# Performance work log

Hardware: AMD Instinct MI355X
Metric: run time of the kernel (lower is better)

The kernel has to match this reference:

```python
import jax, jax.numpy as jnp
import numpy as np


def _cheby_stack(xt, degree):
    # Note: this layer uses T1 = 2*tanh(x) (non-standard), recurrence T_n = 2*xt*T_{n-1} - T_{n-2}
    Ts = [jnp.ones_like(xt)]
    if degree > 0:
        Ts.append(2.0 * xt)
    for n in range(2, degree + 1):
        Ts.append(2.0 * xt * Ts[-1] - Ts[-2])
    return jnp.stack(Ts, axis=2)  # (b, p, n)


def _kan_layer(x, W, tW):
    deg = tW.shape[-1] - 1
    cheby = _cheby_stack(jnp.tanh(x), deg)  # (b, p, n)
    # Fused form of einsum('bpn,qpn->bqp') then einsum('bqp,qp->bq');
    # XLA contracts (tW*W) first, avoiding the huge (b,q,p) intermediate.
    return jnp.einsum('bpn,qpn,qp->bq', cheby, tW, W)


def _cheby_gelu(x, degree=5):
    # Here T1 = tanh(x) (standard), then GeLU(exact) of stacked basis, summed.
    xt = jnp.tanh(x)
    Ts = [jnp.ones_like(xt), xt]
    for n in range(2, degree + 1):
        Ts.append(2.0 * xt * Ts[-1] - Ts[-2])
    st = jnp.stack(Ts, axis=-1)
    return jax.nn.gelu(st, approximate=False).sum(axis=-1)


def setup_inputs() -> dict:
    key = jax.random.key(0)
    ks = jax.random.split(key, 12)
    batch, in_dim, mid, out_dim, deg = 131072, 8, 128, 1, 8
    nfeat = 32
    d = {}
    d['x'] = jax.random.normal(ks[0], (batch, in_dim), jnp.float32)
    d['B'] = jax.random.normal(ks[1], (in_dim, nfeat), jnp.float32)  # scale=1.0
    dims = [(mid, 2 * nfeat), (mid, mid), (mid, mid), (mid, mid), (out_dim, mid)]
    for i, (q, p) in enumerate(dims):
        std_W = np.sqrt(5.0 / (p + q)).astype(np.float32)
        std_tW = np.float32(1.0 / (deg + 1))
        d[f'W{i}'] = std_W * jax.random.normal(ks[2 + 2 * i], (q, p), jnp.float32)
        d[f'tW{i}'] = 0.1 + std_tW * jax.random.normal(ks[3 + 2 * i], (q, p, deg + 1), jnp.float32)
    return d


def reference(x, B, W0, tW0, W1, tW1, W2, tW2, W3, tW3, W4, tW4):
    # FourierFeatures
    proj = (2.0 * jnp.pi) * (x @ B)
    h = jnp.concatenate([jnp.sin(proj), jnp.cos(proj)], axis=-1)  # (b, 64)
    # KAN layers; dropout_prob=0.0 (eval) -> identity. Middle layers get residual
    h = _kan_layer(h, W0, tW0)
    h = _kan_layer(h, W1, tW1) + h
    h = _kan_layer(h, W2, tW2) + h
    h = _kan_layer(h, W3, tW3) + h
    h = _kan_layer(h, W4, tW4)  # (b, 1)
    return _cheby_gelu(h, degree=5)
```

## Files before the change

### kernel.cpp

```cpp
#include <hip/hip_runtime.h>

#define TPB 256

typedef _Float16 f16x8 __attribute__((ext_vector_type(8)));
typedef __fp16 h16x2 __attribute__((ext_vector_type(2)));
typedef float f32x4 __attribute__((ext_vector_type(4)));

static constexpr int WT_L0 = 0;
static constexpr int WT_L1 = 65536;
static constexpr int WT_L2 = 196608;
static constexpr int WT_L3 = 327680;
static constexpr int WT_END = 458752;
static constexpr int F32_BASE = WT_END;
static constexpr int MST = 132;

__device__ __forceinline__ float fast_tanh2(float x) {
  float e = __expf(2.0f * x);
  return fmaf(-4.0f, __builtin_amdgcn_rcpf(e + 1.0f), 2.0f);
}
__device__ __forceinline__ float gelu_exact(float v) {
  return 0.5f * v * (1.0f + erff(v * 0.70710678f));
}

__global__ void fuse_w_f16(const float* __restrict__ W, const float* __restrict__ tW,
                           _Float16* __restrict__ out_hi, _Float16* __restrict__ out_lo,
                           int P, int total, int sbits) {
  int i = blockIdx.x * 256 + threadIdx.x;
  if (i >= total) return;
  int j = i & 7, q = (i >> 3) & 15, g = (i >> 7) & 3, t = (i >> 9) & 7;
  int s = (i >> 12) & ((1 << sbits) - 1);
  int n1 = i >> (12 + sbits);
  int p = s * 32 + g * 8 + j;
  int qg = t * 16 + q;
  float v = tW[(qg * P + p) * 9 + (n1 + 1)] * W[qg * P + p];
  _Float16 hi = (_Float16)v;
  out_hi[i] = hi;
  out_lo[i] = (_Float16)(v - (float)hi);
}
__global__ void fuse_bias(const float* __restrict__ W, const float* __restrict__ tW,
                          float* __restrict__ bias, int P, int Q) {
  int q = blockIdx.x * 64 + threadIdx.x;
  if (q >= Q) return;
  float s = 0.0f;
  for (int p = 0; p < P; ++p) s += tW[(q * P + p) * 9] * W[q * P + p];
  bias[q] = s;
}
__global__ void fuse_w4(const float* __restrict__ W, const float* __restrict__ tW,
                        float* __restrict__ out) {
  int i = blockIdx.x * 128 + threadIdx.x;
  if (i >= 1152) return;
  out[i] = tW[i] * W[i / 9];
}

template <int S, bool RES>
__device__ __forceinline__ void layer_mfma(const float* __restrict__ mT,
                                           const _Float16* __restrict__ wt_hi,
                                           const _Float16* __restrict__ wt_lo,
                                           const float* __restrict__ biasL,
                                           f32x4 (&acc)[4][2], int l, int wq) {
  const int c15 = l & 15, g = l >> 4;
#pragma unroll
  for (int qt = 0; qt < 2; ++qt) {
    float bv = biasL[wq * 32 + qt * 16 + c15];
#pragma unroll
    for (int rt = 0; rt < 4; ++rt)
#pragma unroll
      for (int j = 0; j < 4; ++j) {
        if (RES) acc[rt][qt][j] += bv; else acc[rt][qt][j] = bv;
      }
  }
  const _Float16* slot_hi = wt_hi + wq * 1024 + l * 8;
  const _Float16* slot_lo = wt_lo + wq * 1024 + l * 8;
  float mv[4][8], up[4][8], uc[4][8];
  f16x8 bh0[2], bl0[2], bh1[2], bl1[2];

#define LB(dh, dl, ks)                                                        \
  {                                                                           \
    int s_ = (ks) >> 3, n_ = (ks) & 7;                                        \
    size_t off_ = (size_t)(n_ * S + s_) * 4096;                               \
    _Pragma("unroll") for (int qt = 0; qt < 2; ++qt) {                        \
      dh[qt] = *(const f16x8*)(slot_hi + off_ + qt * 512);                    \
      dl[qt] = *(const f16x8*)(slot_lo + off_ + qt * 512);                    \
    }                                                                         \
  }

#define AREAD(s_)                                                             \
  {                                                                           \
    _Pragma("unroll") for (int rt = 0; rt < 4; ++rt) {                        \
      const f32x4* mp_ =                                                      \
          (const f32x4*)(mT + (rt * 16 + c15) * MST + (s_) * 32 + g * 8);     \
      f32x4 a_ = mp_[0], b_ = mp_[1];                                         \
      _Pragma("unroll") for (int ii = 0; ii < 4; ++ii) {                      \
        mv[rt][ii] = a_[ii]; mv[rt][4 + ii] = b_[ii];                         \
      }                                                                       \
      _Pragma("unroll") for (int ii = 0; ii < 8; ++ii) {                      \
        up[rt][ii] = 1.0f; uc[rt][ii] = mv[rt][ii];                           \
      }                                                                       \
    }                                                                         \
  }

#define STEP(bh, bl)                                                          \
  {                                                                           \
    f16x8 afh[4], afl[4];                                                     \
    _Pragma("unroll") for (int rt = 0; rt < 4; ++rt) {                        \
      union U8 { h16x2 h2[4]; f16x8 v; } uh_, ul_;                            \
      _Pragma("unroll") for (int ii = 0; ii < 4; ++ii) {                      \
        float v0 = uc[rt][2 * ii], v1 = uc[rt][2 * ii + 1];                   \
        h16x2 h_ = __builtin_amdgcn_cvt_pkrtz(v0, v1);                        \
        uh_.h2[ii] = h_;                                                      \
        ul_.h2[ii] = __builtin_amdgcn_cvt_pkrtz(v0 - (float)h_[0],            \
                                                v1 - (float)h_[1]);           \
      }                                                                       \
      afh[rt] = uh_.v; afl[rt] = ul_.v;                                       \
    }                                                                         \
    _Pragma("unroll") for (int rt = 0; rt < 4; ++rt)                          \
      _Pragma("unroll") for (int ii = 0; ii < 8; ++ii) {                      \
        float u_ = fmaf(mv[rt][ii], uc[rt][ii], -up[rt][ii]);                 \
        up[rt][ii] = uc[rt][ii]; uc[rt][ii] = u_;                             \
      }                                                                       \
    _Pragma("unroll") for (int qt = 0; qt < 2; ++qt)                          \
      _Pragma("unroll") for (int rt = 0; rt < 4; ++rt)                        \
        acc[rt][qt] = __builtin_amdgcn_mfma_f32_16x16x32_f16(                 \
            afh[rt], bh[qt], acc[rt][qt], 0, 0, 0);                           \
    _Pragma("unroll") for (int qt = 0; qt < 2; ++qt)                          \
      _Pragma("unroll") for (int rt = 0; rt < 4; ++rt)                        \
        acc[rt][qt] = __builtin_amdgcn_mfma_f32_16x16x32_f16(                 \
            afl[rt], bh[qt], acc[rt][qt], 0, 0, 0);                           \
    _Pragma("unroll") for (int qt = 0; qt < 2; ++qt)                          \
      _Pragma("unroll") for (int rt = 0; rt < 4; ++rt)                        \
        acc[rt][qt] = __builtin_amdgcn_mfma_f32_16x16x32_f16(                 \
            afh[rt], bl[qt], acc[rt][qt], 0, 0, 0);                           \
  }

  LB(bh0, bl0, 0);
#pragma unroll 1
  for (int i = 0; i < 4 * S; ++i) {
    int ks = 2 * i;
    if ((ks & 7) == 0) AREAD(ks >> 3);
    LB(bh1, bl1, ks + 1);
    STEP(bh0, bl0);
    if (ks + 2 < 8 * S) LB(bh0, bl0, ks + 2);
    STEP(bh1, bl1);
  }
#undef LB
#undef AREAD
#undef STEP
}

__device__ __forceinline__ void write_m(float* __restrict__ mT,
                                        const f32x4 (&acc)[4][2], int l, int wq) {
  const int c15 = l & 15, g = l >> 4;
#pragma unroll
  for (int rt = 0; rt < 4; ++rt)
#pragma unroll
    for (int qt = 0; qt < 2; ++qt)
#pragma unroll
      for (int j = 0; j < 4; ++j) {
        int row = rt * 16 + g * 4 + j;
        int col = wq * 32 + qt * 16 + c15;
        mT[row * MST + col] = fast_tanh2(acc[rt][qt][j]);
      }
}

__global__ void __launch_bounds__(TPB, 2)
kan_mfma(const float* __restrict__ x, const float* __restrict__ Bm,
         const _Float16* __restrict__ wt_hi, const _Float16* __restrict__ wt_lo,
         const float* __restrict__ bias, const float* __restrict__ w4,
         float* __restrict__ out) {
  __shared__ float mT[64 * MST];
  int tid = threadIdx.x;
  int l = tid & 63;
  int wq = tid >> 6;
  int row0 = blockIdx.x * 64;

  {
    const float4* xp = (const float4*)(x + (size_t)(row0 + l) * 8);
    float4 a = xp[0], c4 = xp[1];
    float xv[8] = {a.x, a.y, a.z, a.w, c4.x, c4.y, c4.z, c4.w};
#pragma unroll
    for (int jj = 0; jj < 8; ++jj) {
      int j = wq * 8 + jj;
      float pr = 0.0f;
#pragma unroll
      for (int k = 0; k < 8; ++k) pr = fmaf(xv[k], Bm[k * 32 + j], pr);
      float ang = 6.2831853071795864f * pr;
      float sv, cv;
      sincosf(ang, &sv, &cv);
      mT[l * MST + j] = fast_tanh2(sv);
      mT[l * MST + 32 + j] = fast_tanh2(cv);
    }
  }
  __syncthreads();

  f32x4 acc[4][2];
  layer_mfma<2, false>(mT, wt_hi + WT_L0, wt_lo + WT_L0, bias + 0, acc, l, wq);
  __syncthreads();
  write_m(mT, acc, l, wq);
  __syncthreads();
  layer_mfma<4, true>(mT, wt_hi + WT_L1, wt_lo + WT_L1, bias + 128, acc, l, wq);
  __syncthreads();
  write_m(mT, acc, l, wq);
  __syncthreads();
  layer_mfma<4, true>(mT, wt_hi + WT_L2, wt_lo + WT_L2, bias + 256, acc, l, wq);
  __syncthreads();
  write_m(mT, acc, l, wq);
  __syncthreads();
  layer_mfma<4, true>(mT, wt_hi + WT_L3, wt_lo + WT_L3, bias + 384, acc, l, wq);
  __syncthreads();
  write_m(mT, acc, l, wq);
  __syncthreads();

  {
    int r16 = l & 15, pq = l >> 4;
    int r = wq * 16 + r16;
    const float* w4h = w4 + pq * 32 * 9;
    float part = 0.0f;
#pragma unroll 4
    for (int pp = 0; pp < 32; ++pp) {
      float mm = mT[r * MST + pq * 32 + pp];
      const float* wp = w4h + pp * 9;
      part += wp[0];
      part = fmaf(mm, wp[1], part);
      float u2 = 1.0f, u1 = mm;
#pragma unroll
      for (int n = 2; n < 9; ++n) {
        float u = fmaf(mm, u1, -u2);
        u2 = u1;
        u1 = u;
        part = fmaf(u, wp[n], part);
      }
    }
    part += __shfl_xor(part, 16);
    part += __shfl_xor(part, 32);
    if (l < 16) {
      float v = part;
      float t = 0.5f * fast_tanh2(v);
      float m2 = t + t;
      float tm2 = 1.0f, tm1 = t;
      float y = gelu_exact(1.0f) + gelu_exact(t);
#pragma unroll
      for (int n = 2; n <= 5; ++n) {
        float tn = fmaf(m2, tm1, -tm2);
        tm2 = tm1;
        tm1 = tn;
        y += gelu_exact(tn);
      }
      out[row0 + r] = y;
    }
  }
}

extern "C" void kernel_launch(void* const* d_in, const int* in_sizes, int n_in,
                              void* d_out, int out_size, void* d_ws, size_t ws_size,
                              hipStream_t stream) {
  const float* x   = (const float*)d_in[0];
  const float* Bm  = (const float*)d_in[1];
  const float* W0  = (const float*)d_in[2];
  const float* tW0 = (const float*)d_in[3];
  const float* W1  = (const float*)d_in[4];
  const float* tW1 = (const float*)d_in[5];
  const float* W2  = (const float*)d_in[6];
  const float* tW2 = (const float*)d_in[7];
  const float* W3  = (const float*)d_in[8];
  const float* tW3 = (const float*)d_in[9];
  const float* W4  = (const float*)d_in[10];
  const float* tW4 = (const float*)d_in[11];

  _Float16* wt_hi = (_Float16*)d_ws;
  _Float16* wt_lo = wt_hi + WT_END;
  float* fws = (float*)d_ws + F32_BASE;
  float* bias = fws;
  float* w4 = fws + 512;

  fuse_w_f16<<<65536 / 256, 256, 0, stream>>>(W0, tW0, wt_hi + WT_L0, wt_lo + WT_L0, 64, 65536, 1);
  fuse_w_f16<<<131072 / 256, 256, 0, stream>>>(W1, tW1, wt_hi + WT_L1, wt_lo + WT_L1, 128, 131072, 2);
  fuse_w_f16<<<131072 / 256, 256, 0, stream>>>(W2, tW2, wt_hi + WT_L2, wt_lo + WT_L2, 128, 131072, 2);
  fuse_w_f16<<<131072 / 256, 256, 0, stream>>>(W3, tW3, wt_hi + WT_L3, wt_lo + WT_L3, 128, 131072, 2);
  fuse_bias<<<2, 64, 0, stream>>>(W0, tW0, bias + 0, 64, 128);
  fuse_bias<<<2, 64, 0, stream>>>(W1, tW1, bias + 128, 128, 128);
  fuse_bias<<<2, 64, 0, stream>>>(W2, tW2, bias + 256, 128, 128);
  fuse_bias<<<2, 64, 0, stream>>>(W3, tW3, bias + 384, 128, 128);
  fuse_w4<<<9, 128, 0, stream>>>(W4, tW4, w4);

  kan_mfma<<<131072 / 64, TPB, 0, stream>>>(x, Bm, wt_hi, wt_lo, bias, w4, (float*)d_out);
}
```

Measured before the change: 482.7 us.

## Share Chebyshev A-fragment generation across warps via double-buffered LDS

Previously each of the four warps recomputed the full Chebyshev basis and fp16 hi/lo split for all 64 rows, which is 4x redundant VALU work. Now each thread generates one slice of the basis for one chunk, writes the packed hi/lo A fragments to a double-buffered shared-memory buffer, and every warp reads them back for its MFMAs. This adds a block-wide barrier per K-chunk and extra LDS traffic, and drops the register-prefetched weight pipeline. Launch bounds are raised to three blocks per CU to exploit the lower register footprint.

```diff
diff --git a/kernel.cpp b/kernel.cpp
--- a/kernel.cpp
+++ b/kernel.cpp
@@ -52,13 +52,73 @@
   out[i] = tW[i] * W[i / 9];
 }
 
+#define STAGE(k)                                                               \
+  {                                                                            \
+    int s_ = (k) >> 3, n1_ = (k) & 7, bf_ = (k) & 1;                           \
+    if (n1_ == 0) {                                                            \
+      const f32x4* mp_ = (const f32x4*)(mT + wrow * MST + s_ * 32 + wg * 8);   \
+      f32x4 a_ = mp_[0], b_ = mp_[1];                                          \
+      _Pragma("unroll") for (int i = 0; i < 4; ++i) {                          \
+        mv[i] = a_[i]; mv[4 + i] = b_[i];                                      \
+      }                                                                        \
+      _Pragma("unroll") for (int i = 0; i < 8; ++i) {                          \
+        up[i] = 1.0f; uc[i] = mv[i];                                           \
+      }                                                                        \
+    } else {                                                                   \
+      _Pragma("unroll") for (int i = 0; i < 8; ++i) {                          \
+        float u_ = fmaf(mv[i], uc[i], -up[i]);                                 \
+        up[i] = uc[i]; uc[i] = u_;                                             \
+      }                                                                        \
+    }                                                                          \
+    union UU { h16x2 h2[4]; f16x8 v; } uh_, ul_;                               \
+    _Pragma("unroll") for (int ii = 0; ii < 4; ++ii) {                         \
+      float v0 = uc[2 * ii], v1 = uc[2 * ii + 1];                              \
+      h16x2 h_ = __builtin_amdgcn_cvt_pkrtz(v0, v1);                           \
+      uh_.h2[ii] = h_;                                                         \
+      ul_.h2[ii] =                                                             \
+          __builtin_amdgcn_cvt_pkrtz(v0 - (float)h_[0], v1 - (float)h_[1]);    \
+    }                                                                          \
+    *(f16x8*)&abuf[bf_][wrt][0][wslot * 8] = uh_.v;                            \
+    *(f16x8*)&abuf[bf_][wrt][1][wslot * 8] = ul_.v;                            \
+  }
+
+#define CONSUME(k)                                                             \
+  {                                                                            \
+    int s_ = (k) >> 3, n1_ = (k) & 7, bf_ = (k) & 1;                           \
+    size_t toff_ = (size_t)(n1_ * S + s_) * 4096 + wq * 1024 + l * 8;          \
+    f16x8 bh_[2], bl_[2];                                                      \
+    bh_[0] = *(const f16x8*)(wt_hi + toff_);                                   \
+    bh_[1] = *(const f16x8*)(wt_hi + toff_ + 512);                             \
+    bl_[0] = *(const f16x8*)(wt_lo + toff_);                                   \
+    bl_[1] = *(const f16x8*)(wt_lo + toff_ + 512);                             \
+    f16x8 ah_[4], al_[4];                                                      \
+    _Pragma("unroll") for (int rt = 0; rt < 4; ++rt) {                         \
+      ah_[rt] = *(const f16x8*)&abuf[bf_][rt][0][l * 8];                       \
+      al_[rt] = *(const f16x8*)&abuf[bf_][rt][1][l * 8];                       \
+    }                                                                          \
+    _Pragma("unroll") for (int qt = 0; qt < 2; ++qt)                           \
+      _Pragma("unroll") for (int rt = 0; rt < 4; ++rt)                         \
+          acc[rt][qt] = __builtin_amdgcn_mfma_f32_16x16x32_f16(                \
+              ah_[rt], bh_[qt], acc[rt][qt], 0, 0, 0);                         \
+    _Pragma("unroll") for (int qt = 0; qt < 2; ++qt)                           \
+      _Pragma("unroll") for (int rt = 0; rt < 4; ++rt)                         \
+          acc[rt][qt] = __builtin_amdgcn_mfma_f32_16x16x32_f16(                \
+              al_[rt], bh_[qt], acc[rt][qt], 0, 0, 0);                         \
+    _Pragma("unroll") for (int qt = 0; qt < 2; ++qt)                           \
+      _Pragma("unroll") for (int rt = 0; rt < 4; ++rt)                         \
+          acc[rt][qt] = __builtin_amdgcn_mfma_f32_16x16x32_f16(                \
+              ah_[rt], bl_[qt], acc[rt][qt], 0, 0, 0);                         \
+  }
+
 template <int S, bool RES>
-__device__ __forceinline__ void layer_mfma(const float* __restrict__ mT,
+__device__ __forceinline__ void layer_coop(float* __restrict__ mT,
+                                           _Float16 (*abuf)[4][2][512],
                                            const _Float16* __restrict__ wt_hi,
                                            const _Float16* __restrict__ wt_lo,
                                            const float* __restrict__ biasL,
-                                           f32x4 (&acc)[4][2], int l, int wq) {
-  const int c15 = l & 15, g = l >> 4;
+                                           f32x4 (&acc)[4][2], int l, int wq,
+                                           int wrow, int wg, int wrt, int wslot) {
+  const int c15 = l & 15;
 #pragma unroll
   for (int qt = 0; qt < 2; ++qt) {
     float bv = biasL[wq * 32 + qt * 16 + c15];
@@ -69,82 +129,16 @@
         if (RES) acc[rt][qt][j] += bv; else acc[rt][qt][j] = bv;
       }
   }
-  const _Float16* slot_hi = wt_hi + wq * 1024 + l * 8;
-  const _Float16* slot_lo = wt_lo + wq * 1024 + l * 8;
-  float mv[4][8], up[4][8], uc[4][8];
-  f16x8 bh0[2], bl0[2], bh1[2], bl1[2];
-
-#define LB(dh, dl, ks)                                                        \
-  {                                                                           \
-    int s_ = (ks) >> 3, n_ = (ks) & 7;                                        \
-    size_t off_ = (size_t)(n_ * S + s_) * 4096;                               \
-    _Pragma("unroll") for (int qt = 0; qt < 2; ++qt) {                        \
-      dh[qt] = *(const f16x8*)(slot_hi + off_ + qt * 512);                    \
-      dl[qt] = *(const f16x8*)(slot_lo + off_ + qt * 512);                    \
-    }                                                                         \
-  }
-
-#define AREAD(s_)                                                             \
-  {                                                                           \
-    _Pragma("unroll") for (int rt = 0; rt < 4; ++rt) {                        \
-      const f32x4* mp_ =                                                      \
-          (const f32x4*)(mT + (rt * 16 + c15) * MST + (s_) * 32 + g * 8);     \
-      f32x4 a_ = mp_[0], b_ = mp_[1];                                         \
-      _Pragma("unroll") for (int ii = 0; ii < 4; ++ii) {                      \
-        mv[rt][ii] = a_[ii]; mv[rt][4 + ii] = b_[ii];                         \
-      }                                                                       \
-      _Pragma("unroll") for (int ii = 0; ii < 8; ++ii) {                      \
-        up[rt][ii] = 1.0f; uc[rt][ii] = mv[rt][ii];                           \
-      }                                                                       \
-    }                                                                         \
-  }
-
-#define STEP(bh, bl)                                                          \
-  {                                                                           \
-    f16x8 afh[4], afl[4];                                                     \
-    _Pragma("unroll") for (int rt = 0; rt < 4; ++rt) {                        \
-      union U8 { h16x2 h2[4]; f16x8 v; } uh_, ul_;                            \
-      _Pragma("unroll") for (int ii = 0; ii < 4; ++ii) {                      \
-        float v0 = uc[rt][2 * ii], v1 = uc[rt][2 * ii + 1];                   \
-        h16x2 h_ = __builtin_amdgcn_cvt_pkrtz(v0, v1);                        \
-        uh_.h2[ii] = h_;                                                      \
-        ul_.h2[ii] = __builtin_amdgcn_cvt_pkrtz(v0 - (float)h_[0],            \
-                                                v1 - (float)h_[1]);           \
-      }                                                                       \
-      afh[rt] = uh_.v; afl[rt] = ul_.v;                                       \
-    }                                                                         \
-    _Pragma("unroll") for (int rt = 0; rt < 4; ++rt)                          \
-      _Pragma("unroll") for (int ii = 0; ii < 8; ++ii) {                      \
-        float u_ = fmaf(mv[rt][ii], uc[rt][ii], -up[rt][ii]);                 \
-        up[rt][ii] = uc[rt][ii]; uc[rt][ii] = u_;                             \
-      }                                                                       \
-    _Pragma("unroll") for (int qt = 0; qt < 2; ++qt)                          \
-      _Pragma("unroll") for (int rt = 0; rt < 4; ++rt)                        \
-        acc[rt][qt] = __builtin_amdgcn_mfma_f32_16x16x32_f16(                 \
-            afh[rt], bh[qt], acc[rt][qt], 0, 0, 0);                           \
-    _Pragma("unroll") for (int qt = 0; qt < 2; ++qt)                          \
-      _Pragma("unroll") for (int rt = 0; rt < 4; ++rt)                        \
-        acc[rt][qt] = __builtin_amdgcn_mfma_f32_16x16x32_f16(                 \
-            afl[rt], bh[qt], acc[rt][qt], 0, 0, 0);                           \
-    _Pragma("unroll") for (int qt = 0; qt < 2; ++qt)                          \
-      _Pragma("unroll") for (int rt = 0; rt < 4; ++rt)                        \
-        acc[rt][qt] = __builtin_amdgcn_mfma_f32_16x16x32_f16(                 \
-            afh[rt], bl[qt], acc[rt][qt], 0, 0, 0);                           \
-  }
-
-  LB(bh0, bl0, 0);
+  float mv[8], up[8], uc[8];
+  constexpr int NCH = 8 * S;
+  STAGE(0)
+  __syncthreads();
 #pragma unroll 1
-  for (int i = 0; i < 4 * S; ++i) {
-    int ks = 2 * i;
-    if ((ks & 7) == 0) AREAD(ks >> 3);
-    LB(bh1, bl1, ks + 1);
-    STEP(bh0, bl0);
-    if (ks + 2 < 8 * S) LB(bh0, bl0, ks + 2);
-    STEP(bh1, bl1);
-  }
-#undef LB
-#undef AREAD
-#undef STEP
+  for (int k = 0; k < NCH; ++k) {
+    if (k + 1 < NCH) STAGE(k + 1)
+    CONSUME(k)
+    __syncthreads();
+  }
 }
 
 __device__ __forceinline__ void write_m(float* __restrict__ mT,
@@ -162,15 +156,20 @@
       }
 }
 
-__global__ void __launch_bounds__(TPB, 2)
+__global__ void __launch_bounds__(TPB, 3)
 kan_mfma(const float* __restrict__ x, const float* __restrict__ Bm,
          const _Float16* __restrict__ wt_hi, const _Float16* __restrict__ wt_lo,
          const float* __restrict__ bias, const float* __restrict__ w4,
          float* __restrict__ out) {
   __shared__ float mT[64 * MST];
+  __shared__ __align__(16) _Float16 abuf[2][4][2][512];
   int tid = threadIdx.x;
   int l = tid & 63;
   int wq = tid >> 6;
+  int wrow = tid >> 2;
+  int wg = tid & 3;
+  int wrt = wrow >> 4;
+  int wslot = wg * 16 + (wrow & 15);
   int row0 = blockIdx.x * 64;
 
   {
@@ -193,20 +192,16 @@
   __syncthreads();
 
   f32x4 acc[4][2];
-  layer_mfma<2, false>(mT, wt_hi + WT_L0, wt_lo + WT_L0, bias + 0, acc, l, wq);
-  __syncthreads();
-  write_m(mT, acc, l, wq);
-  __syncthreads();
-  layer_mfma<4, true>(mT, wt_hi + WT_L1, wt_lo + WT_L1, bias + 128, acc, l, wq);
-  __syncthreads();
-  write_m(mT, acc, l, wq);
-  __syncthreads();
-  layer_mfma<4, true>(mT, wt_hi + WT_L2, wt_lo + WT_L2, bias + 256, acc, l, wq);
-  __syncthreads();
-  write_m(mT, acc, l, wq);
-  __syncthreads();
-  layer_mfma<4, true>(mT, wt_hi + WT_L3, wt_lo + WT_L3, bias + 384, acc, l, wq);
-  __syncthreads();
+  layer_coop<2, false>(mT, abuf, wt_hi + WT_L0, wt_lo + WT_L0, bias + 0, acc, l, wq, wrow, wg, wrt, wslot);
+  write_m(mT, acc, l, wq);
+  __syncthreads();
+  layer_coop<4, true>(mT, abuf, wt_hi + WT_L1, wt_lo + WT_L1, bias + 128, acc, l, wq, wrow, wg, wrt, wslot);
+  write_m(mT, acc, l, wq);
+  __syncthreads();
+  layer_coop<4, true>(mT, abuf, wt_hi + WT_L2, wt_lo + WT_L2, bias + 256, acc, l, wq, wrow, wg, wrt, wslot);
+  write_m(mT, acc, l, wq);
+  __syncthreads();
+  layer_coop<4, true>(mT, abuf, wt_hi + WT_L3, wt_lo + WT_L3, bias + 384, acc, l, wq, wrow, wg, wrt, wslot);
   write_m(mT, acc, l, wq);
   __syncthreads();
 
```

Result: faster. 411.5 us (-14.8%).
